# Optimization experiments

Measured on AMD Instinct MI355X. Metric: run time of the kernel, lower is better.

## Reference

```python
import jax, jax.numpy as jnp
import numpy as np

DIM = 1024
DEPTH = 2
D_STATE = 16
EXPAND = 2            # standard Mamba expand factor -> d_inner = 2*dim
D_CONV = 4
DT_RANK = DIM // 16   # ceil(dim/16) = 64
D_INNER = DIM * EXPAND
BATCH = 2
SEQ = 1024


def setup_inputs() -> dict:
    key = jax.random.key(0)
    ks = jax.random.split(key, 8)
    def n(k, shape, scale):
        return jax.random.normal(k, shape, jnp.float32) * scale
    # A_log initialized as log(1..N) per channel (S4D-real init, as in mamba_ssm)
    A_log = jnp.tile(jnp.log(jnp.arange(1, D_STATE + 1, dtype=jnp.float32))[None, None, :],
                     (DEPTH, D_INNER, 1))
    return {
        "x": n(ks[0], (BATCH, SEQ, DIM), 1.0),
        "in_proj_w": n(ks[1], (DEPTH, 2 * D_INNER, DIM), DIM ** -0.5),
        "conv_w": n(ks[2], (DEPTH, D_INNER, D_CONV), D_CONV ** -0.5),
        "conv_b": jnp.zeros((DEPTH, D_INNER), jnp.float32),
        "x_proj_w": n(ks[3], (DEPTH, DT_RANK + 2 * D_STATE, D_INNER), D_INNER ** -0.5),
        "dt_proj_w": n(ks[4], (DEPTH, D_INNER, DT_RANK), DT_RANK ** -0.5),
        "dt_proj_b": n(ks[5], (DEPTH, D_INNER), 0.1),
        "A_log": A_log,
        "D": jnp.ones((DEPTH, D_INNER), jnp.float32),
        "out_proj_w": n(ks[6], (DEPTH, DIM, D_INNER), D_INNER ** -0.5),
    }


def _mamba_layer(x, in_w, cw, cb, xp_w, dtw, dtb, A_log, Dp, ow):
    # x: [B, L, dim]
    Bsz = x.shape[0]
    xz = jnp.einsum('bld,ed->ble', x, in_w)            # [B, L, 2*d_inner]
    xi, z = jnp.split(xz, 2, axis=-1)
    # causal depthwise conv1d over time
    xc = jnp.transpose(xi, (0, 2, 1))                  # [B, d_inner, L]
    xc = jax.lax.conv_general_dilated(xc, cw[:, None, :], (1,), [(D_CONV - 1, 0)],
                                      feature_group_count=D_INNER)
    xc = xc + cb[None, :, None]
    xc = jax.nn.silu(jnp.transpose(xc, (0, 2, 1)))     # [B, L, d_inner]
    # input-dependent dt, B, C
    x_dbl = jnp.einsum('bld,ed->ble', xc, xp_w)        # [B, L, dt_rank+2*N]
    dt_raw = x_dbl[..., :DT_RANK]
    Bm = x_dbl[..., DT_RANK:DT_RANK + D_STATE]         # [B, L, N]
    Cm = x_dbl[..., DT_RANK + D_STATE:]                # [B, L, N]
    dt = jax.nn.softplus(jnp.einsum('blr,dr->bld', dt_raw, dtw) + dtb)  # [B, L, d_inner]
    A = -jnp.exp(A_log)                                # [d_inner, N]
    dA = jnp.exp(dt[..., None] * A[None, None])        # [B, L, d_inner, N]
    dBu = dt[..., None] * Bm[:, :, None, :] * xc[..., None]

    def step(h, inp):
        dA_t, dBu_t, C_t = inp
        h = dA_t * h + dBu_t                           # [B, d_inner, N]
        y = jnp.einsum('bdn,bn->bd', h, C_t)
        return h, y

    h0 = jnp.zeros((Bsz, D_INNER, D_STATE), x.dtype)
    _, ys = jax.lax.scan(step, h0,
                         (dA.transpose(1, 0, 2, 3), dBu.transpose(1, 0, 2, 3),
                          Cm.transpose(1, 0, 2)))
    y = ys.transpose(1, 0, 2) + Dp[None, None, :] * xc
    y = y * jax.nn.silu(z)
    return jnp.einsum('bld,od->blo', y, ow)


def reference(x, in_proj_w, conv_w, conv_b, x_proj_w, dt_proj_w, dt_proj_b, A_log, D, out_proj_w):
    for i in range(DEPTH):
        x = _mamba_layer(x, in_proj_w[i], conv_w[i], conv_b[i], x_proj_w[i],
                         dt_proj_w[i], dt_proj_b[i], A_log[i], D[i], out_proj_w[i])
    return x
```

## Files before the change

kernel.cpp:

```cpp
#include <hip/hip_runtime.h>
#include <hip/hip_bf16.h>

typedef __hip_bfloat16 bf16;
typedef __attribute__((ext_vector_type(8))) short short8;
typedef __attribute__((ext_vector_type(4))) short shortx4;
typedef __attribute__((ext_vector_type(4))) float floatx4;

#define BATCH   2
#define SEQ     1024
#define DIM     1024
#define D_INNER 2048
#define D_STATE 16
#define DT_RANK 64
#define MROWS   (BATCH * SEQ)
#define CHUNK   32
#define NCHUNK  (SEQ / CHUNK)

__device__ __forceinline__ float bf2f(bf16 x) { return __bfloat162float(x); }
__device__ __forceinline__ bf16  f2bf(float x) { return __float2bfloat16(x); }
__device__ __forceinline__ short bfbits(float x) {
    bf16 b = __float2bfloat16(x); short s; __builtin_memcpy(&s, &b, 2); return s;
}

__device__ __forceinline__ void ld_lds16(const void* g, void* l) {
    __builtin_amdgcn_global_load_lds(
        (const __attribute__((address_space(1))) void*)g,
        (__attribute__((address_space(3))) void*)l, 16, 0, 0);
}

__device__ __forceinline__ void cast4(const float* in, short* o, int i) {
    floatx4 v = ((const floatx4*)in)[i];
    shortx4 r;
    r.x = bfbits(v.x); r.y = bfbits(v.y); r.z = bfbits(v.z); r.w = bfbits(v.w);
    ((shortx4*)o)[i] = r;
}
__global__ __launch_bounds__(256) void cast_k(
    const float* __restrict__ in, short* __restrict__ o, int n4)
{
    int i = blockIdx.x * 256 + threadIdx.x;
    if (i < n4) cast4(in, o, i);
}
__global__ __launch_bounds__(256) void cast2_k(
    const float* __restrict__ a, short* __restrict__ oa, int na4,
    const float* __restrict__ b, short* __restrict__ ob, int nb4)
{
    int i = blockIdx.x * 256 + threadIdx.x;
    if (i < na4) cast4(a, oa, i);
    else if (i - na4 < nb4) cast4(b, ob, i - na4);
}

__device__ __forceinline__ short8 ld8_any(const void* p, size_t eoff, int is_f32) {
    if (is_f32) {
        const float* f = (const float*)p + eoff;
        floatx4 a = *(const floatx4*)f;
        floatx4 b = *(const floatx4*)(f + 4);
        short8 r;
        r[0] = bfbits(a[0]); r[1] = bfbits(a[1]); r[2] = bfbits(a[2]); r[3] = bfbits(a[3]);
        r[4] = bfbits(b[0]); r[5] = bfbits(b[1]); r[6] = bfbits(b[2]); r[7] = bfbits(b[3]);
        return r;
    } else {
        return *(const short8*)((const bf16*)p + eoff);
    }
}

__global__ __launch_bounds__(256) void gemm128(
    const bf16* __restrict__ A, int lda,
    const bf16* __restrict__ B, int ldb,
    float* __restrict__ Cf, bf16* __restrict__ Cb, int ldc,
    int kchunk, size_t psize)
{
    __shared__ short As[128 * 32];
    __shared__ short Bs[128 * 32];
    const int tid  = threadIdx.x;
    const int wave = tid >> 6;
    const int lane = tid & 63;
    const int m0 = blockIdx.y * 128;
    const int n0 = blockIdx.x * 128;
    const int wm = (wave & 1) * 64;
    const int wn = (wave >> 1) * 64;
    const int r16  = lane & 15;
    const int quad = lane >> 4;
    const int r0 = tid >> 2;
    const int c0 = (tid & 3) << 3;
    const int kbeg = blockIdx.z * kchunk;

    floatx4 acc[4][4] = {};

    for (int k0 = kbeg; k0 < kbeg + kchunk; k0 += 32) {
        __syncthreads();
        ld_lds16(A + (size_t)(m0 + r0) * lda + k0 + c0,      As + tid * 8);
        ld_lds16(A + (size_t)(m0 + r0 + 64) * lda + k0 + c0, As + (tid + 256) * 8);
        ld_lds16(B + (size_t)(n0 + r0) * ldb + k0 + c0,      Bs + tid * 8);
        ld_lds16(B + (size_t)(n0 + r0 + 64) * ldb + k0 + c0, Bs + (tid + 256) * 8);
        __syncthreads();
        short8 af[4], bg[4];
#pragma unroll
        for (int i = 0; i < 4; i++) {
            af[i] = *(const short8*)(As + (wm + i * 16 + r16) * 32 + quad * 8);
            bg[i] = *(const short8*)(Bs + (wn + i * 16 + r16) * 32 + quad * 8);
        }
#pragma unroll
        for (int i = 0; i < 4; i++)
#pragma unroll
            for (int j = 0; j < 4; j++)
                acc[i][j] = __builtin_amdgcn_mfma_f32_16x16x32_bf16(af[i], bg[j], acc[i][j], 0, 0, 0);
    }

    float* Cfp = Cf ? Cf + (size_t)blockIdx.z * psize : nullptr;
#pragma unroll
    for (int i = 0; i < 4; i++)
#pragma unroll
        for (int j = 0; j < 4; j++) {
            int gm = m0 + wm + i * 16 + quad * 4;
            int gn = n0 + wn + j * 16 + r16;
#pragma unroll
            for (int r = 0; r < 4; r++) {
                size_t o = (size_t)(gm + r) * ldc + gn;
                float v = acc[i][j][r];
                if (Cfp) Cfp[o] = v;
                if (Cb) Cb[o] = f2bf(v);
            }
        }
}

__global__ __launch_bounds__(256) void gemm_bt(
    const void* __restrict__ A, int a_f32, int lda,
    const void* __restrict__ B, int b_f32, int ldb,
    float* __restrict__ Cf, bf16* __restrict__ Cb, int ldc,
    int N, int K, size_t psize,
    const float* __restrict__ bias, int act)
{
    __shared__ short As[64][40];
    __shared__ short Bs[64][40];
    const int m0   = blockIdx.y * 64;
    const int n0   = blockIdx.x * 64;
    const int tid  = threadIdx.x;
    const int wave = tid >> 6;
    const int lane = tid & 63;
    const int srow = tid >> 2;
    const int scol = (tid & 3) << 3;
    const int r16  = lane & 15;
    const int quad = lane >> 4;
    const int kbeg = blockIdx.z * K;

    floatx4 acc[4] = {};

    for (int k0 = kbeg; k0 < kbeg + K; k0 += 32) {
        short8 av = ld8_any(A, (size_t)(m0 + srow) * lda + k0 + scol, a_f32);
        short8 bv = {};
        int gn = n0 + srow;
        if (gn < N) bv = ld8_any(B, (size_t)gn * ldb + k0 + scol, b_f32);
        *(short8*)(&As[srow][scol]) = av;
        *(short8*)(&Bs[srow][scol]) = bv;
        __syncthreads();
        short8 af = *(const short8*)(&As[wave * 16 + r16][quad * 8]);
#pragma unroll
        for (int nt = 0; nt < 4; nt++) {
            short8 bq = *(const short8*)(&Bs[nt * 16 + r16][quad * 8]);
            acc[nt] = __builtin_amdgcn_mfma_f32_16x16x32_bf16(af, bq, acc[nt], 0, 0, 0);
        }
        __syncthreads();
    }

    float* Cfp = Cf ? Cf + (size_t)blockIdx.z * psize : nullptr;
#pragma unroll
    for (int nt = 0; nt < 4; nt++) {
        int gn = n0 + nt * 16 + r16;
        if (gn >= N) continue;
        float bsv = bias ? bias[gn] : 0.f;
#pragma unroll
        for (int r = 0; r < 4; r++) {
            int gm = m0 + wave * 16 + quad * 4 + r;
            float v = acc[nt][r] + bsv;
            if (act == 1) v = (v > 20.f) ? v : log1pf(__expf(v));
            size_t o = (size_t)gm * ldc + gn;
            if (Cfp) Cfp[o] = v;
            if (Cb) Cb[o] = f2bf(v);
        }
    }
}

__global__ __launch_bounds__(256) void reduce8_k(
    const float* __restrict__ part, float* __restrict__ o, int n, size_t psize)
{
    int i = blockIdx.x * 256 + threadIdx.x;
    if (i >= n) return;
    float v = 0.f;
#pragma unroll
    for (int j = 0; j < 8; j++) v += part[i + (size_t)j * psize];
    o[i] = v;
}

__global__ __launch_bounds__(256) void reduce2_k(
    const float* __restrict__ part, size_t psize, int n,
    float* __restrict__ of, bf16* __restrict__ ob)
{
    int i = blockIdx.x * 256 + threadIdx.x;
    if (i >= n) return;
    float v = part[i] + part[i + psize];
    if (of) of[i] = v;
    if (ob) ob[i] = f2bf(v);
}

__global__ __launch_bounds__(256) void conv_silu_k(
    const bf16* __restrict__ xz, const float* __restrict__ cw,
    const float* __restrict__ cb, bf16* __restrict__ xcb)
{
    int idx = blockIdx.x * 256 + threadIdx.x;
    int d   = idx & (D_INNER - 1);
    int bt  = idx >> 11;
    int t   = bt & (SEQ - 1);
    float s = cb[d];
#pragma unroll
    for (int j = 0; j < 4; j++) {
        int tt = t - 3 + j;
        if (tt >= 0) s += cw[d * 4 + j] * bf2f(xz[(size_t)(bt - 3 + j) * 4096 + d]);
    }
    float sig = 1.f / (1.f + __expf(-s));
    xcb[idx] = f2bf(s * sig);
}

__global__ __launch_bounds__(256) void scan1_k(
    const float* __restrict__ dtf, const bf16* __restrict__ xcb,
    const float* __restrict__ xdbl, const float* __restrict__ Alog,
    float* __restrict__ chunk_sdt, float* __restrict__ chunk_S)
{
    __shared__ float dt_s[CHUNK][256];
    __shared__ short xc_s[CHUNK][256];
    __shared__ float B_s[CHUNK][16];
    const int tid = threadIdx.x;
    const int d0  = blockIdx.x * 256;
    const int d   = d0 + tid;
    const int b   = blockIdx.y;
    const int c   = blockIdx.z;
    const size_t rbase = (size_t)b * SEQ + c * CHUNK;

#pragma unroll 4
    for (int t = 0; t < CHUNK; t++) {
        dt_s[t][tid] = dtf[(rbase + t) * D_INNER + d0 + tid];
        ((short*)xc_s)[t * 256 + tid] = *(const short*)&xcb[(rbase + t) * D_INNER + d0 + tid];
    }
    for (int e = tid; e < CHUNK * 16; e += 256) {
        int t = e >> 4, n = e & 15;
        B_s[t][n] = xdbl[(rbase + t) * 96 + 64 + n];
    }
    float A[16];
#pragma unroll
    for (int n = 0; n < 16; n++) A[n] = -__expf(Alog[(size_t)d * 16 + n]);
    float h[16] = {};
    float sdt = 0.f;
    __syncthreads();

    for (int t = 0; t < CHUNK; t++) {
        float dtv = dt_s[t][tid];
        bf16 xcr; short xs = xc_s[t][tid]; __builtin_memcpy(&xcr, &xs, 2);
        float u = dtv * bf2f(xcr);
        sdt += dtv;
        floatx4 B0 = *(const floatx4*)&B_s[t][0];
        floatx4 B1 = *(const floatx4*)&B_s[t][4];
        floatx4 B2 = *(const floatx4*)&B_s[t][8];
        floatx4 B3 = *(const floatx4*)&B_s[t][12];
#pragma unroll
        for (int n = 0; n < 4; n++) {
            h[n]      = __expf(dtv * A[n])      * h[n]      + u * B0[n];
            h[n + 4]  = __expf(dtv * A[n + 4])  * h[n + 4]  + u * B1[n];
            h[n + 8]  = __expf(dtv * A[n + 8])  * h[n + 8]  + u * B2[n];
            h[n + 12] = __expf(dtv * A[n + 12]) * h[n + 12] + u * B3[n];
        }
    }
    chunk_sdt[(b * NCHUNK + c) * D_INNER + d] = sdt;
#pragma unroll
    for (int n = 0; n < 16; n++)
        chunk_S[((size_t)(b * NCHUNK + c) * 16 + n) * D_INNER + d] = h[n];
}

__global__ __launch_bounds__(256) void scanpre_k(
    const float* __restrict__ Alog, const float* __restrict__ chunk_sdt,
    float* __restrict__ chunk_S)
{
    const int d = blockIdx.x * 256 + threadIdx.x;
    const int b = blockIdx.y;
    const int n = blockIdx.z;
    const float Av = -__expf(Alog[(size_t)d * 16 + n]);
    float h = 0.f;
    for (int j = 0; j < NCHUNK; j++) {
        size_t si = ((size_t)(b * NCHUNK + j) * 16 + n) * D_INNER + d;
        float S   = chunk_S[si];
        float sdt = chunk_sdt[(b * NCHUNK + j) * D_INNER + d];
        chunk_S[si] = h;
        h = __expf(sdt * Av) * h + S;
    }
}

__global__ __launch_bounds__(256) void scan2_k(
    const float* __restrict__ dtf, const bf16* __restrict__ xcb,
    const float* __restrict__ xdbl, const bf16* __restrict__ xz,
    const float* __restrict__ Alog, const float* __restrict__ Dp,
    const float* __restrict__ chunk_S, bf16* __restrict__ yb)
{
    __shared__ float dt_s[CHUNK][256];
    __shared__ short xc_s[CHUNK][256];
    __shared__ float B_s[CHUNK][16];
    __shared__ float C_s[CHUNK][16];
    const int tid = threadIdx.x;
    const int d0  = blockIdx.x * 256;
    const int d   = d0 + tid;
    const int b   = blockIdx.y;
    const int c   = blockIdx.z;
    const size_t rbase = (size_t)b * SEQ + c * CHUNK;

#pragma unroll 4
    for (int t = 0; t < CHUNK; t++) {
        dt_s[t][tid] = dtf[(rbase + t) * D_INNER + d0 + tid];
        ((short*)xc_s)[t * 256 + tid] = *(const short*)&xcb[(rbase + t) * D_INNER + d0 + tid];
    }
    for (int e = tid; e < CHUNK * 16; e += 256) {
        int t = e >> 4, n = e & 15;
        B_s[t][n] = xdbl[(rbase + t) * 96 + 64 + n];
        C_s[t][n] = xdbl[(rbase + t) * 96 + 80 + n];
    }
    float A[16];
#pragma unroll
    for (int n = 0; n < 16; n++) A[n] = -__expf(Alog[(size_t)d * 16 + n]);

    float h[16];
#pragma unroll
    for (int n = 0; n < 16; n++)
        h[n] = chunk_S[((size_t)(b * NCHUNK + c) * 16 + n) * D_INNER + d];

    const float Dv = Dp[d];
    __syncthreads();

    for (int t = 0; t < CHUNK; t++) {
        size_t row = rbase + t;
        float dtv = dt_s[t][tid];
        bf16 xcr; short xs = xc_s[t][tid]; __builtin_memcpy(&xcr, &xs, 2);
        float xcv = bf2f(xcr);
        float u = dtv * xcv;
        floatx4 B0 = *(const floatx4*)&B_s[t][0];
        floatx4 B1 = *(const floatx4*)&B_s[t][4];
        floatx4 B2 = *(const floatx4*)&B_s[t][8];
        floatx4 B3 = *(const floatx4*)&B_s[t][12];
        floatx4 C0 = *(const floatx4*)&C_s[t][0];
        floatx4 C1 = *(const floatx4*)&C_s[t][4];
        floatx4 C2 = *(const floatx4*)&C_s[t][8];
        floatx4 C3 = *(const floatx4*)&C_s[t][12];
        float y = 0.f;
#pragma unroll
        for (int n = 0; n < 4; n++) {
            h[n]      = __expf(dtv * A[n])      * h[n]      + u * B0[n];
            h[n + 4]  = __expf(dtv * A[n + 4])  * h[n + 4]  + u * B1[n];
            h[n + 8]  = __expf(dtv * A[n + 8])  * h[n + 8]  + u * B2[n];
            h[n + 12] = __expf(dtv * A[n + 12]) * h[n + 12] + u * B3[n];
            y += h[n] * C0[n] + h[n + 4] * C1[n] + h[n + 8] * C2[n] + h[n + 12] * C3[n];
        }
        float zv = bf2f(xz[row * 4096 + 2048 + d]);
        y = (y + Dv * xcv) * (zv / (1.f + __expf(-zv)));
        yb[row * D_INNER + d] = f2bf(y);
    }
}

extern "C" void kernel_launch(void* const* d_in, const int* in_sizes, int n_in,
                              void* d_out, int out_size, void* d_ws, size_t ws_size,
                              hipStream_t stream)
{
    const float* x    = (const float*)d_in[0];
    const float* inw  = (const float*)d_in[1];
    const float* cw   = (const float*)d_in[2];
    const float* cb   = (const float*)d_in[3];
    const float* xpw  = (const float*)d_in[4];
    const float* dtw  = (const float*)d_in[5];
    const float* dtb  = (const float*)d_in[6];
    const float* Alog = (const float*)d_in[7];
    const float* Dp   = (const float*)d_in[8];
    const float* ow   = (const float*)d_in[9];
    float* out = (float*)d_out;

    char* p = (char*)d_ws;
    bf16*  xzb   = (bf16*)p;  p += (size_t)MROWS * 4096 * 2;
    bf16*  xcb   = (bf16*)p;  p += (size_t)MROWS * D_INNER * 2;
    float* xdblf = (float*)p; p += (size_t)MROWS * 96 * 4;
    float* dtf   = (float*)p; p += (size_t)MROWS * D_INNER * 4;
    bf16*  ybf   = (bf16*)p;  p += (size_t)MROWS * D_INNER * 2;
    bf16*  xmid  = (bf16*)p;  p += (size_t)MROWS * DIM * 2;
    float* csdt  = (float*)p; p += (size_t)BATCH * NCHUNK * D_INNER * 4;
    float* cS    = (float*)p; p += (size_t)BATCH * NCHUNK * 16 * D_INNER * 4;
    bf16*  xb    = (bf16*)p;  p += (size_t)MROWS * DIM * 2;
    bf16*  inwb  = (bf16*)p;  p += (size_t)2 * D_INNER * DIM * 2;
    bf16*  owb   = (bf16*)p;  p += (size_t)DIM * D_INNER * 2;
    float* xprt  = (float*)p; p += (size_t)8 * MROWS * 96 * 4;

    const size_t xp_psize = (size_t)MROWS * 96;
    const size_t op_psize = (size_t)MROWS * DIM;
    float* outp = dtf;

    cast_k<<<(MROWS * DIM / 4 + 255) / 256, 256, 0, stream>>>(x, (short*)xb, MROWS * DIM / 4);

    for (int l = 0; l < 2; l++) {
        const float* xpw_l = xpw + (size_t)l * 96 * D_INNER;
        const float* dtw_l = dtw + (size_t)l * D_INNER * DT_RANK;
        const float* Al    = Alog + (size_t)l * D_INNER * D_STATE;

        {
            int na4 = 2 * D_INNER * DIM / 4, nb4 = DIM * D_INNER / 4;
            cast2_k<<<(na4 + nb4 + 255) / 256, 256, 0, stream>>>(
                inw + (size_t)l * 2 * D_INNER * DIM, (short*)inwb, na4,
                ow + (size_t)l * DIM * D_INNER, (short*)owb, nb4);
        }

        gemm128<<<dim3(32, 16, 1), 256, 0, stream>>>(
            (l == 0) ? xb : xmid, DIM, inwb, DIM,
            nullptr, xzb, 4096, DIM, 0);

        conv_silu_k<<<(MROWS * D_INNER) / 256, 256, 0, stream>>>(
            xzb, cw + (size_t)l * D_INNER * 4, cb + (size_t)l * D_INNER, xcb);

        gemm_bt<<<dim3(2, 32, 8), 256, 0, stream>>>(
            xcb, 0, D_INNER, xpw_l, 1, D_INNER,
            xprt, nullptr, 96, 96, 256, xp_psize, nullptr, 0);
        reduce8_k<<<(MROWS * 96 + 255) / 256, 256, 0, stream>>>(
            xprt, xdblf, MROWS * 96, xp_psize);

        gemm_bt<<<dim3(32, 32), 256, 0, stream>>>(
            xdblf, 1, 96, dtw_l, 1, DT_RANK,
            dtf, nullptr, D_INNER, D_INNER, DT_RANK, 0,
            dtb + (size_t)l * D_INNER, 1);

        scan1_k<<<dim3(D_INNER / 256, BATCH, NCHUNK), 256, 0, stream>>>(
            dtf, xcb, xdblf, Al, csdt, cS);
        scanpre_k<<<dim3(D_INNER / 256, BATCH, D_STATE), 256, 0, stream>>>(
            Al, csdt, cS);
        scan2_k<<<dim3(D_INNER / 256, BATCH, NCHUNK), 256, 0, stream>>>(
            dtf, xcb, xdblf, xzb, Al, Dp + (size_t)l * D_INNER, cS, ybf);

        gemm128<<<dim3(8, 16, 2), 256, 0, stream>>>(
            ybf, D_INNER, owb, D_INNER,
            outp, nullptr, DIM, D_INNER / 2, op_psize);
        reduce2_k<<<(MROWS * DIM + 255) / 256, 256, 0, stream>>>(
            outp, op_psize, MROWS * DIM,
            (l == 1) ? out : nullptr, (l == 0) ? xmid : nullptr);
    }
}
```

Baseline: 445.7 us.

## Fuse chunked scan stages into one cooperative kernel and swizzle GEMM LDS

The three scan kernels (per-chunk state, cross-chunk prefix, output pass) become one cooperative kernel that uses grid.sync between phases. This keeps the dt/xc/B/C tiles in LDS across phases and saves two launches. The GEMM shared-memory tiles get an XOR swizzle on the k-column offset to reduce LDS bank conflicts on the fragment reads. The cost is two grid-wide barriers, and it requires all 512 blocks to be co-resident, which cooperative launch enforces.

Result: slower. 844.2 us (+89.4%).

```diff
diff --git a/kernel.cpp b/kernel.cpp
--- a/kernel.cpp
+++ b/kernel.cpp
@@ -1,5 +1,8 @@
 #include <hip/hip_runtime.h>
 #include <hip/hip_bf16.h>
+#include <hip/hip_cooperative_groups.h>
+
+namespace cg = cooperative_groups;
 
 typedef __hip_bfloat16 bf16;
 typedef __attribute__((ext_vector_type(8))) short short8;
@@ -81,7 +84,8 @@
     const int r16  = lane & 15;
     const int quad = lane >> 4;
     const int r0 = tid >> 2;
-    const int c0 = (tid & 3) << 3;
+    const int sw = (r0 & 3) ^ ((r0 >> 2) & 3);
+    const int c0 = (((tid & 3) ^ sw) << 3);
     const int kbeg = blockIdx.z * kchunk;
 
     floatx4 acc[4][4] = {};
@@ -96,8 +100,12 @@
         short8 af[4], bg[4];
 #pragma unroll
         for (int i = 0; i < 4; i++) {
-            af[i] = *(const short8*)(As + (wm + i * 16 + r16) * 32 + quad * 8);
-            bg[i] = *(const short8*)(Bs + (wn + i * 16 + r16) * 32 + quad * 8);
+            int Ra = wm + i * 16 + r16;
+            int Rb = wn + i * 16 + r16;
+            int sa = (Ra & 3) ^ ((Ra >> 2) & 3);
+            int sb = (Rb & 3) ^ ((Rb >> 2) & 3);
+            af[i] = *(const short8*)(As + Ra * 32 + ((quad ^ sa) << 3));
+            bg[i] = *(const short8*)(Bs + Rb * 32 + ((quad ^ sb) << 3));
         }
 #pragma unroll
         for (int i = 0; i < 4; i++)
@@ -220,83 +228,12 @@
     xcb[idx] = f2bf(s * sig);
 }
 
-__global__ __launch_bounds__(256) void scan1_k(
-    const float* __restrict__ dtf, const bf16* __restrict__ xcb,
-    const float* __restrict__ xdbl, const float* __restrict__ Alog,
-    float* __restrict__ chunk_sdt, float* __restrict__ chunk_S)
-{
-    __shared__ float dt_s[CHUNK][256];
-    __shared__ short xc_s[CHUNK][256];
-    __shared__ float B_s[CHUNK][16];
-    const int tid = threadIdx.x;
-    const int d0  = blockIdx.x * 256;
-    const int d   = d0 + tid;
-    const int b   = blockIdx.y;
-    const int c   = blockIdx.z;
-    const size_t rbase = (size_t)b * SEQ + c * CHUNK;
-
-#pragma unroll 4
-    for (int t = 0; t < CHUNK; t++) {
-        dt_s[t][tid] = dtf[(rbase + t) * D_INNER + d0 + tid];
-        ((short*)xc_s)[t * 256 + tid] = *(const short*)&xcb[(rbase + t) * D_INNER + d0 + tid];
-    }
-    for (int e = tid; e < CHUNK * 16; e += 256) {
-        int t = e >> 4, n = e & 15;
-        B_s[t][n] = xdbl[(rbase + t) * 96 + 64 + n];
-    }
-    float A[16];
-#pragma unroll
-    for (int n = 0; n < 16; n++) A[n] = -__expf(Alog[(size_t)d * 16 + n]);
-    float h[16] = {};
-    float sdt = 0.f;
-    __syncthreads();
-
-    for (int t = 0; t < CHUNK; t++) {
-        float dtv = dt_s[t][tid];
-        bf16 xcr; short xs = xc_s[t][tid]; __builtin_memcpy(&xcr, &xs, 2);
-        float u = dtv * bf2f(xcr);
-        sdt += dtv;
-        floatx4 B0 = *(const floatx4*)&B_s[t][0];
-        floatx4 B1 = *(const floatx4*)&B_s[t][4];
-        floatx4 B2 = *(const floatx4*)&B_s[t][8];
-        floatx4 B3 = *(const floatx4*)&B_s[t][12];
-#pragma unroll
-        for (int n = 0; n < 4; n++) {
-            h[n]      = __expf(dtv * A[n])      * h[n]      + u * B0[n];
-            h[n + 4]  = __expf(dtv * A[n + 4])  * h[n + 4]  + u * B1[n];
-            h[n + 8]  = __expf(dtv * A[n + 8])  * h[n + 8]  + u * B2[n];
-            h[n + 12] = __expf(dtv * A[n + 12]) * h[n + 12] + u * B3[n];
-        }
-    }
-    chunk_sdt[(b * NCHUNK + c) * D_INNER + d] = sdt;
-#pragma unroll
-    for (int n = 0; n < 16; n++)
-        chunk_S[((size_t)(b * NCHUNK + c) * 16 + n) * D_INNER + d] = h[n];
-}
-
-__global__ __launch_bounds__(256) void scanpre_k(
-    const float* __restrict__ Alog, const float* __restrict__ chunk_sdt,
-    float* __restrict__ chunk_S)
-{
-    const int d = blockIdx.x * 256 + threadIdx.x;
-    const int b = blockIdx.y;
-    const int n = blockIdx.z;
-    const float Av = -__expf(Alog[(size_t)d * 16 + n]);
-    float h = 0.f;
-    for (int j = 0; j < NCHUNK; j++) {
-        size_t si = ((size_t)(b * NCHUNK + j) * 16 + n) * D_INNER + d;
-        float S   = chunk_S[si];
-        float sdt = chunk_sdt[(b * NCHUNK + j) * D_INNER + d];
-        chunk_S[si] = h;
-        h = __expf(sdt * Av) * h + S;
-    }
-}
-
-__global__ __launch_bounds__(256) void scan2_k(
+__global__ __launch_bounds__(256) void scan_fused_k(
     const float* __restrict__ dtf, const bf16* __restrict__ xcb,
     const float* __restrict__ xdbl, const bf16* __restrict__ xz,
     const float* __restrict__ Alog, const float* __restrict__ Dp,
-    const float* __restrict__ chunk_S, bf16* __restrict__ yb)
+    float* __restrict__ csdt, float* __restrict__ cS,
+    bf16* __restrict__ yb)
 {
     __shared__ float dt_s[CHUNK][256];
     __shared__ short xc_s[CHUNK][256];
@@ -308,6 +245,7 @@
     const int b   = blockIdx.y;
     const int c   = blockIdx.z;
     const size_t rbase = (size_t)b * SEQ + c * CHUNK;
+    cg::grid_group grid = cg::this_grid();
 
 #pragma unroll 4
     for (int t = 0; t < CHUNK; t++) {
@@ -322,14 +260,60 @@
     float A[16];
 #pragma unroll
     for (int n = 0; n < 16; n++) A[n] = -__expf(Alog[(size_t)d * 16 + n]);
-
-    float h[16];
+    float h[16] = {};
+    float sdt = 0.f;
+    __syncthreads();
+
+    for (int t = 0; t < CHUNK; t++) {
+        float dtv = dt_s[t][tid];
+        bf16 xcr; short xs = xc_s[t][tid]; __builtin_memcpy(&xcr, &xs, 2);
+        float u = dtv * bf2f(xcr);
+        sdt += dtv;
+        floatx4 B0 = *(const floatx4*)&B_s[t][0];
+        floatx4 B1 = *(const floatx4*)&B_s[t][4];
+        floatx4 B2 = *(const floatx4*)&B_s[t][8];
+        floatx4 B3 = *(const floatx4*)&B_s[t][12];
+#pragma unroll
+        for (int n = 0; n < 4; n++) {
+            h[n]      = __expf(dtv * A[n])      * h[n]      + u * B0[n];
+            h[n + 4]  = __expf(dtv * A[n + 4])  * h[n + 4]  + u * B1[n];
+            h[n + 8]  = __expf(dtv * A[n + 8])  * h[n + 8]  + u * B2[n];
+            h[n + 12] = __expf(dtv * A[n + 12]) * h[n + 12] + u * B3[n];
+        }
+    }
+    csdt[(b * NCHUNK + c) * D_INNER + d] = sdt;
 #pragma unroll
     for (int n = 0; n < 16; n++)
-        h[n] = chunk_S[((size_t)(b * NCHUNK + c) * 16 + n) * D_INNER + d];
-
+        cS[((size_t)(b * NCHUNK + c) * 16 + n) * D_INNER + d] = h[n];
+    __threadfence();
+    grid.sync();
+
+    {
+        int lb = blockIdx.x + 8 * (blockIdx.y + 2 * blockIdx.z);
+        int gid = lb * 256 + tid;
+        if (gid < BATCH * D_INNER * D_STATE) {
+            int dd = gid & (D_INNER - 1);
+            int nn = (gid >> 11) & 15;
+            int bb = gid >> 15;
+            float Av = -__expf(Alog[(size_t)dd * 16 + nn]);
+            float hh = 0.f;
+#pragma unroll 4
+            for (int j = 0; j < NCHUNK; j++) {
+                size_t si = ((size_t)(bb * NCHUNK + j) * 16 + nn) * D_INNER + dd;
+                float S  = cS[si];
+                float sd = csdt[(bb * NCHUNK + j) * D_INNER + dd];
+                cS[si] = hh;
+                hh = __expf(sd * Av) * hh + S;
+            }
+        }
+    }
+    __threadfence();
+    grid.sync();
+
+#pragma unroll
+    for (int n = 0; n < 16; n++)
+        h[n] = cS[((size_t)(b * NCHUNK + c) * 16 + n) * D_INNER + d];
     const float Dv = Dp[d];
-    __syncthreads();
 
     for (int t = 0; t < CHUNK; t++) {
         size_t row = rbase + t;
@@ -400,6 +384,7 @@
         const float* xpw_l = xpw + (size_t)l * 96 * D_INNER;
         const float* dtw_l = dtw + (size_t)l * D_INNER * DT_RANK;
         const float* Al    = Alog + (size_t)l * D_INNER * D_STATE;
+        const float* Dpl   = Dp + (size_t)l * D_INNER;
 
         {
             int na4 = 2 * D_INNER * DIM / 4, nb4 = DIM * D_INNER / 4;
@@ -426,12 +411,15 @@
             dtf, nullptr, D_INNER, D_INNER, DT_RANK, 0,
             dtb + (size_t)l * D_INNER, 1);
 
-        scan1_k<<<dim3(D_INNER / 256, BATCH, NCHUNK), 256, 0, stream>>>(
-            dtf, xcb, xdblf, Al, csdt, cS);
-        scanpre_k<<<dim3(D_INNER / 256, BATCH, D_STATE), 256, 0, stream>>>(
-            Al, csdt, cS);
-        scan2_k<<<dim3(D_INNER / 256, BATCH, NCHUNK), 256, 0, stream>>>(
-            dtf, xcb, xdblf, xzb, Al, Dp + (size_t)l * D_INNER, cS, ybf);
+        {
+            void* args[] = {
+                (void*)&dtf, (void*)&xcb, (void*)&xdblf, (void*)&xzb,
+                (void*)&Al, (void*)&Dpl, (void*)&csdt, (void*)&cS, (void*)&ybf
+            };
+            hipLaunchCooperativeKernel((void*)scan_fused_k,
+                dim3(D_INNER / 256, BATCH, NCHUNK), dim3(256),
+                args, 0, stream);
+        }
 
         gemm128<<<dim3(8, 16, 2), 256, 0, stream>>>(
             ybf, D_INNER, owb, D_INNER,
```
